# Performance work log

Hardware: AMD Instinct MI355X
Metric: run time of the kernel (lower is better)

The kernel has to match this reference:

```python
import jax, jax.numpy as jnp
import numpy as np

D_MODEL = 1024
NUM_HEADS = 16
D_K = D_MODEL // NUM_HEADS
B, S = 4, 2048


def setup_inputs() -> dict:
    key = jax.random.key(0)
    ks = jax.random.split(key, 11)
    scale = 1.0 / np.sqrt(D_MODEL)
    inp = {
        "query": jax.random.normal(ks[0], (B, S, D_MODEL), dtype=jnp.float32),
        "key": jax.random.normal(ks[1], (B, S, D_MODEL), dtype=jnp.float32),
        "value": jax.random.normal(ks[2], (B, S, D_MODEL), dtype=jnp.float32),
        "w_q": jax.random.normal(ks[3], (D_MODEL, D_MODEL), dtype=jnp.float32) * scale,
        "b_q": jnp.zeros((D_MODEL,), dtype=jnp.float32),
        "w_k": jax.random.normal(ks[4], (D_MODEL, D_MODEL), dtype=jnp.float32) * scale,
        "b_k": jnp.zeros((D_MODEL,), dtype=jnp.float32),
        "w_v": jax.random.normal(ks[5], (D_MODEL, D_MODEL), dtype=jnp.float32) * scale,
        "b_v": jnp.zeros((D_MODEL,), dtype=jnp.float32),
        "w_o": jax.random.normal(ks[6], (D_MODEL, D_MODEL), dtype=jnp.float32) * scale,
        "b_o": jnp.zeros((D_MODEL,), dtype=jnp.float32),
    }
    return inp


def reference(query, key, value, w_q, b_q, w_k, b_k, w_v, b_v, w_o, b_o):
    # Linear projections; torch Linear computes x @ W.T + b, here w_* stored as (out, in)
    def proj(x, w, b):
        y = jnp.einsum("bsd,ed->bse", x, w) + b
        # [B, S, D] -> [B, H, S, d_k]
        return y.reshape(B, S, NUM_HEADS, D_K).transpose(0, 2, 1, 3)

    Q = proj(query, w_q, b_q)
    K = proj(key, w_k, b_k)
    V = proj(value, w_v, b_v)

    scores = jnp.einsum("bhqd,bhkd->bhqk", Q, K) / jnp.sqrt(jnp.float32(D_K))
    weights = jax.nn.softmax(scores, axis=-1)
    attn = jnp.einsum("bhqk,bhkd->bhqd", weights, V)  # [B, H, S, d_k]
    attn = attn.transpose(0, 2, 1, 3).reshape(B, S, D_MODEL)
    return jnp.einsum("bsd,ed->bse", attn, w_o) + b_o
```

## Files before the change

kernel.cpp:

```cpp
#include <hip/hip_runtime.h>
#include <hip/hip_bf16.h>

#define D_MODEL 1024
#define NHEADS 16
#define DKH 64
#define BATCH 4
#define SEQ 2048
#define MROWS (BATCH*SEQ)
#define BSD ((size_t)MROWS * D_MODEL)
#define WSZ ((size_t)D_MODEL * D_MODEL)
#define LOG2E 1.4426950408889634f
#define NT2 (SEQ/32)

typedef __attribute__((ext_vector_type(8)))  short   s16x8;
typedef __attribute__((ext_vector_type(8)))  __bf16  bf16x8;
typedef __attribute__((ext_vector_type(4)))  __bf16  bf16x4;
typedef __attribute__((ext_vector_type(4)))  float   f32x4;
typedef __attribute__((ext_vector_type(16))) float   f32x16;

#define SWZ(row, scol) ((((int)(row)) << 6) + (((int)(scol)) ^ ((((int)(row)) & 7) << 3)))
#define SWZV(row, scol) ((((int)(row)) << 5) + (((int)(scol)) ^ (((((int)(row)) >> 1) & 3) << 3)))

__device__ inline short f2bf(float f) {
    __bf16 h = (__bf16)f;
    short s; __builtin_memcpy(&s, &h, 2); return s;
}

__device__ inline unsigned pk2(float a, float b) {
    unsigned r;
    asm("v_cvt_pk_bf16_f32 %0, %1, %2" : "=v"(r) : "v"(a), "v"(b));
    return r;
}
__device__ inline bf16x8 mk8(unsigned w0, unsigned w1, unsigned w2, unsigned w3) {
    union { unsigned u[4]; bf16x8 v; } x;
    x.u[0] = w0; x.u[1] = w1; x.u[2] = w2; x.u[3] = w3;
    return x.v;
}

__device__ inline void gl_lds16(const void* g, void* l) {
    __builtin_amdgcn_global_load_lds(
        (const __attribute__((address_space(1))) unsigned*)g,
        (__attribute__((address_space(3))) unsigned*)l, 16, 0, 0);
}

struct CvtPtrs { const float* src[7]; short* dst[7]; };

__global__ __launch_bounds__(256) void cvt_all(CvtPtrs p)
{
    const int bx = blockIdx.x;
    int buf, boff;
    if (bx < 3 * 4096) { buf = bx >> 12; boff = bx & 4095; }
    else { const int r = bx - 3 * 4096; buf = 3 + (r >> 9); boff = r & 511; }
    const float* __restrict__ src = p.src[buf];
    short* __restrict__ dst = p.dst[buf];
    const size_t i = ((size_t)boff * 256 + threadIdx.x) * 8;
    const float4 a = *(const float4*)(src + i);
    const float4 b = *(const float4*)(src + i + 4);
    s16x8 v;
    v[0]=f2bf(a.x); v[1]=f2bf(a.y); v[2]=f2bf(a.z); v[3]=f2bf(a.w);
    v[4]=f2bf(b.x); v[5]=f2bf(b.y); v[6]=f2bf(b.z); v[7]=f2bf(b.w);
    *(s16x8*)(dst + i) = v;
}

__device__ __forceinline__ void gemm_body(
    const short* __restrict__ A, const short* __restrict__ W,
    const float* __restrict__ bias, void* __restrict__ Cout, float scale,
    int omode)
{
    __shared__ __align__(16) short As[128 * 64];
    __shared__ __align__(16) short Bs[128 * 64];
    const int t   = threadIdx.x;
    const int l   = t & 63;
    const int wid = t >> 6;
    const int g   = l >> 4, r16 = l & 15;
    const int wm  = wid >> 1, wn = wid & 1;
    const int bid = blockIdx.x + (blockIdx.y << 3);
    const int swz = (bid & 7) * 64 + (bid >> 3);
    const int n0  = (swz & 7) * 128, m0 = (swz >> 3) * 128;
    const int srow = t >> 3;
    const int scol = (t & 7) * 8;

    f32x4 acc[4][4];
    #pragma unroll
    for (int mi = 0; mi < 4; ++mi)
        #pragma unroll
        for (int ni = 0; ni < 4; ++ni)
            acc[mi][ni] = (f32x4)0.0f;

    const short* Ap = A + (size_t)(m0 + srow) * D_MODEL + scol;
    const short* Wp = W + (size_t)(n0 + srow) * D_MODEL + scol;
    short* AsW = As + wid * 512;
    short* BsW = Bs + wid * 512;

    for (int k0 = 0; k0 < D_MODEL; k0 += 64) {
        #pragma unroll
        for (int p = 0; p < 4; ++p) {
            gl_lds16(Ap + (size_t)p * 32 * D_MODEL + k0, AsW + p * 2048);
            gl_lds16(Wp + (size_t)p * 32 * D_MODEL + k0, BsW + p * 2048);
        }
        __syncthreads();
        #pragma unroll
        for (int kc = 0; kc < 2; ++kc) {
            bf16x8 a[4], b[4];
            #pragma unroll
            for (int mi = 0; mi < 4; ++mi)
                a[mi] = *(const bf16x8*)&As[(wm * 64 + mi * 16 + r16) * 64 + kc * 32 + g * 8];
            #pragma unroll
            for (int ni = 0; ni < 4; ++ni)
                b[ni] = *(const bf16x8*)&Bs[(wn * 64 + ni * 16 + r16) * 64 + kc * 32 + g * 8];
            #pragma unroll
            for (int mi = 0; mi < 4; ++mi)
                #pragma unroll
                for (int ni = 0; ni < 4; ++ni)
                    acc[mi][ni] = __builtin_amdgcn_mfma_f32_16x16x32_bf16(a[mi], b[ni], acc[mi][ni], 0, 0, 0);
        }
        __syncthreads();
    }

    #pragma unroll
    for (int mi = 0; mi < 4; ++mi)
        #pragma unroll
        for (int ni = 0; ni < 4; ++ni) {
            const int n  = n0 + wn * 64 + ni * 16 + r16;
            const int mB = m0 + wm * 64 + mi * 16 + g * 4;
            float v[4];
            #pragma unroll
            for (int j = 0; j < 4; ++j)
                v[j] = (acc[mi][ni][j] + bias[n]) * scale;
            if (omode == 0) {
                #pragma unroll
                for (int j = 0; j < 4; ++j)
                    ((float*)Cout)[(size_t)(mB + j) * D_MODEL + n] = v[j];
            } else if (omode == 1) {
                const size_t base = ((size_t)((mB >> 11) * NHEADS + (n >> 6)) << 11);
                #pragma unroll
                for (int j = 0; j < 4; ++j)
                    ((short*)Cout)[(base + ((mB + j) & 2047)) * DKH + (n & 63)] = f2bf(v[j]);
            } else {
                bf16x4 ov;
                ov[0] = (__bf16)v[0]; ov[1] = (__bf16)v[1];
                ov[2] = (__bf16)v[2]; ov[3] = (__bf16)v[3];
                const size_t row = (size_t)((mB >> 11) * NHEADS + (n >> 6)) * DKH + (n & 63);
                *(bf16x4*)&((short*)Cout)[row * SEQ + (mB & 2047)] = ov;
            }
        }
}

struct QkvArgs {
    const short* A[3]; const short* W[3]; const float* bias[3];
    short* out[3]; float scale[3]; int omode[3];
};

__global__ __launch_bounds__(256, 2) void gemm_qkv(QkvArgs q) {
    const int z = blockIdx.z;
    gemm_body(q.A[z], q.W[z], q.bias[z], q.out[z], q.scale[z], q.omode[z]);
}

__global__ __launch_bounds__(256, 2) void gemm_out(
    const short* A, const short* W, const float* bias, float* C) {
    gemm_body(A, W, bias, C, 1.0f, 0);
}

__global__ __launch_bounds__(256, 2) void attn_mfma(
    const short* __restrict__ Qg, const short* __restrict__ Kg,
    const short* __restrict__ Vtg, short* __restrict__ Ab)
{
    __shared__ __align__(16) short lds[24576];
    const int t   = threadIdx.x;
    const int l   = t & 63;
    const int wid = t >> 6;
    const int l31 = l & 31, hi = l >> 5;
    const int bid  = blockIdx.x + (blockIdx.y << 3);
    const int swz  = (bid & 7) * 64 + (bid >> 3);
    const int head = swz >> 3, b = head >> 4, h = head & 15;
    const int q0   = (swz & 7) << 8;
    const int wq0  = wid * 64;

    const short* Kbase = Kg  + (size_t)head * SEQ * DKH;
    const short* Vbase = Vtg + (size_t)head * DKH * SEQ;

    const int qrow = t >> 3;
    const int qg8  = ((t & 7) ^ (qrow & 7)) * 8;
    const short* qsrc = Qg + ((size_t)head * SEQ + q0 + qrow) * DKH + qg8;
    const int krow = t >> 3;
    const short* ksrc = Kbase + (size_t)krow * DKH + (((t & 7) ^ (krow & 7)) * 8);
    const int vrow = t >> 2;
    const short* vsrc = Vbase + (size_t)vrow * SEQ + (((t & 3) ^ ((vrow >> 1) & 3)) * 8);

    short* const ldsQ  = &lds[wid * 512];
    short* const ldsKA = &lds[16384 + wid * 512];
    short* const ldsVA = &lds[18432 + wid * 512];
    short* const ldsKB = &lds[20480 + wid * 512];
    short* const ldsVB = &lds[22528 + wid * 512];

    #pragma unroll
    for (int i = 0; i < 8; ++i)
        gl_lds16(qsrc + (size_t)i * 32 * DKH, ldsQ + i * 2048);
    gl_lds16(ksrc, ldsKA);
    gl_lds16(vsrc, ldsVA);
    gl_lds16(ksrc + 2048, ldsKB);
    gl_lds16(vsrc + 32,   ldsVB);
    __syncthreads();

    bf16x8 bq0[4], bq1[4];
    #pragma unroll
    for (int kc = 0; kc < 4; ++kc) {
        bq0[kc] = *(const bf16x8*)&lds[SWZ(wq0 + l31,      kc * 16 + hi * 8)];
        bq1[kc] = *(const bf16x8*)&lds[SWZ(wq0 + 32 + l31, kc * 16 + hi * 8)];
    }

    f32x16 o00 = (f32x16)0.0f, o01 = (f32x16)0.0f;
    f32x16 o10 = (f32x16)0.0f, o11 = (f32x16)0.0f;
    float l0 = 0.0f, l1 = 0.0f;

    for (int kt = 0; kt < NT2; ++kt) {
        const int KO = (kt & 1) ? 20480 : 16384;
        const int VO = (kt & 1) ? 22528 : 18432;

        f32x16 s0 = (f32x16)0.0f, s1 = (f32x16)0.0f;
        __builtin_amdgcn_s_setprio(1);
        #pragma unroll
        for (int kc = 0; kc < 4; ++kc) {
            const bf16x8 ak = *(const bf16x8*)&lds[KO + SWZ(l31, kc * 16 + hi * 8)];
            s0 = __builtin_amdgcn_mfma_f32_32x32x16_bf16(ak, bq0[kc], s0, 0, 0, 0);
            s1 = __builtin_amdgcn_mfma_f32_32x32x16_bf16(ak, bq1[kc], s1, 0, 0, 0);
        }
        __builtin_amdgcn_s_setprio(0);

        #pragma unroll
        for (int r = 0; r < 16; ++r) s0[r] = __builtin_amdgcn_exp2f(s0[r]);
        #pragma unroll
        for (int r = 0; r < 16; ++r) s1[r] = __builtin_amdgcn_exp2f(s1[r]);
        {
            const float a0 = (s0[0]+s0[1]) + (s0[2]+s0[3]);
            const float a1 = (s0[4]+s0[5]) + (s0[6]+s0[7]);
            const float a2 = (s0[8]+s0[9]) + (s0[10]+s0[11]);
            const float a3 = (s0[12]+s0[13]) + (s0[14]+s0[15]);
            l0 += (a0 + a1) + (a2 + a3);
            const float c0 = (s1[0]+s1[1]) + (s1[2]+s1[3]);
            const float c1 = (s1[4]+s1[5]) + (s1[6]+s1[7]);
            const float c2 = (s1[8]+s1[9]) + (s1[10]+s1[11]);
            const float c3 = (s1[12]+s1[13]) + (s1[14]+s1[15]);
            l1 += (c0 + c1) + (c2 + c3);
        }

        bf16x8 bp00, bp01, bp10, bp11;
        {
            unsigned a0 = pk2(s0[0], s0[1]),  b0 = pk2(s0[4],  s0[5]);
            unsigned a1 = pk2(s0[2], s0[3]),  b1 = pk2(s0[6],  s0[7]);
            asm("v_permlane32_swap_b32 %0, %1" : "+v"(a0), "+v"(b0));
            asm("v_permlane32_swap_b32 %0, %1" : "+v"(a1), "+v"(b1));
            bp00 = mk8(a0, a1, b0, b1);
            unsigned a2 = pk2(s0[8], s0[9]),   b2 = pk2(s0[12], s0[13]);
            unsigned a3 = pk2(s0[10], s0[11]), b3 = pk2(s0[14], s0[15]);
            asm("v_permlane32_swap_b32 %0, %1" : "+v"(a2), "+v"(b2));
            asm("v_permlane32_swap_b32 %0, %1" : "+v"(a3), "+v"(b3));
            bp01 = mk8(a2, a3, b2, b3);
        }
        {
            unsigned a0 = pk2(s1[0], s1[1]),  b0 = pk2(s1[4],  s1[5]);
            unsigned a1 = pk2(s1[2], s1[3]),  b1 = pk2(s1[6],  s1[7]);
            asm("v_permlane32_swap_b32 %0, %1" : "+v"(a0), "+v"(b0));
            asm("v_permlane32_swap_b32 %0, %1" : "+v"(a1), "+v"(b1));
            bp10 = mk8(a0, a1, b0, b1);
            unsigned a2 = pk2(s1[8], s1[9]),   b2 = pk2(s1[12], s1[13]);
            unsigned a3 = pk2(s1[10], s1[11]), b3 = pk2(s1[14], s1[15]);
            asm("v_permlane32_swap_b32 %0, %1" : "+v"(a2), "+v"(b2));
            asm("v_permlane32_swap_b32 %0, %1" : "+v"(a3), "+v"(b3));
            bp11 = mk8(a2, a3, b2, b3);
        }

        __builtin_amdgcn_s_setprio(1);
        {
            const bf16x8 avA0 = *(const bf16x8*)&lds[VO + SWZV(l31,      hi * 8)];
            const bf16x8 avA1 = *(const bf16x8*)&lds[VO + SWZV(32 + l31, hi * 8)];
            o00 = __builtin_amdgcn_mfma_f32_32x32x16_bf16(avA0, bp00, o00, 0, 0, 0);
            o01 = __builtin_amdgcn_mfma_f32_32x32x16_bf16(avA1, bp00, o01, 0, 0, 0);
            o10 = __builtin_amdgcn_mfma_f32_32x32x16_bf16(avA0, bp10, o10, 0, 0, 0);
            o11 = __builtin_amdgcn_mfma_f32_32x32x16_bf16(avA1, bp10, o11, 0, 0, 0);
            const bf16x8 avB0 = *(const bf16x8*)&lds[VO + SWZV(l31,      16 + hi * 8)];
            const bf16x8 avB1 = *(const bf16x8*)&lds[VO + SWZV(32 + l31, 16 + hi * 8)];
            o00 = __builtin_amdgcn_mfma_f32_32x32x16_bf16(avB0, bp01, o00, 0, 0, 0);
            o01 = __builtin_amdgcn_mfma_f32_32x32x16_bf16(avB1, bp01, o01, 0, 0, 0);
            o10 = __builtin_amdgcn_mfma_f32_32x32x16_bf16(avB0, bp11, o10, 0, 0, 0);
            o11 = __builtin_amdgcn_mfma_f32_32x32x16_bf16(avB1, bp11, o11, 0, 0, 0);
        }
        __builtin_amdgcn_s_setprio(0);

        __syncthreads();
        if (kt + 2 < NT2) {
            gl_lds16(ksrc + (size_t)(kt + 2) * 2048, (kt & 1) ? ldsKB : ldsKA);
            gl_lds16(vsrc + (kt + 2) * 32,           (kt & 1) ? ldsVB : ldsVA);
        }
    }

    #pragma unroll
    for (int qb = 0; qb < 2; ++qb) {
        const float lr = qb ? l1 : l0;
        const f32x16 oa = qb ? o10 : o00;
        const f32x16 ob = qb ? o11 : o01;
        const float lt = lr + __shfl_xor(lr, 32);
        const float inv = 1.0f / lt;
        const int q = q0 + wq0 + qb * 32 + l31;
        short* Op = Ab + ((size_t)b * SEQ + q) * D_MODEL + h * DKH;
        #pragma unroll
        for (int rr = 0; rr < 4; ++rr) {
            bf16x4 ov;
            ov[0] = (__bf16)(oa[rr*4+0] * inv); ov[1] = (__bf16)(oa[rr*4+1] * inv);
            ov[2] = (__bf16)(oa[rr*4+2] * inv); ov[3] = (__bf16)(oa[rr*4+3] * inv);
            *(bf16x4*)&Op[rr * 8 + hi * 4] = ov;
            bf16x4 ow;
            ow[0] = (__bf16)(ob[rr*4+0] * inv); ow[1] = (__bf16)(ob[rr*4+1] * inv);
            ow[2] = (__bf16)(ob[rr*4+2] * inv); ow[3] = (__bf16)(ob[rr*4+3] * inv);
            *(bf16x4*)&Op[32 + rr * 8 + hi * 4] = ow;
        }
    }
}

extern "C" void kernel_launch(void* const* d_in, const int* in_sizes, int n_in,
                              void* d_out, int out_size, void* d_ws, size_t ws_size,
                              hipStream_t stream) {
    const float* q_in = (const float*)d_in[0];
    const float* k_in = (const float*)d_in[1];
    const float* v_in = (const float*)d_in[2];
    const float* w_q  = (const float*)d_in[3];
    const float* b_q  = (const float*)d_in[4];
    const float* w_k  = (const float*)d_in[5];
    const float* b_k  = (const float*)d_in[6];
    const float* w_v  = (const float*)d_in[7];
    const float* b_v  = (const float*)d_in[8];
    const float* w_o  = (const float*)d_in[9];
    const float* b_o  = (const float*)d_in[10];
    float* out = (float*)d_out;

    short* ws = (short*)d_ws;
    short* Qc = ws;
    short* Kc = ws + BSD;
    short* Vc = ws + 2 * BSD;
    short* Wq = ws + 3 * BSD;
    short* Wk = Wq + WSZ;
    short* Wv = Wk + WSZ;
    short* Wo = Wv + WSZ;
    short* Qb = ws + 3 * BSD + 4 * WSZ;
    short* Kb = Qb + BSD;
    short* Vt = Kb + BSD;
    short* Ab = Kc;

    dim3 blk(256);

    CvtPtrs cp;
    cp.src[0] = q_in; cp.dst[0] = Qc;
    cp.src[1] = k_in; cp.dst[1] = Kc;
    cp.src[2] = v_in; cp.dst[2] = Vc;
    cp.src[3] = w_q;  cp.dst[3] = Wq;
    cp.src[4] = w_k;  cp.dst[4] = Wk;
    cp.src[5] = w_v;  cp.dst[5] = Wv;
    cp.src[6] = w_o;  cp.dst[6] = Wo;
    cvt_all<<<dim3(3 * 4096 + 4 * 512), blk, 0, stream>>>(cp);

    QkvArgs qa;
    qa.A[0] = Qc; qa.W[0] = Wq; qa.bias[0] = b_q; qa.out[0] = Qb; qa.scale[0] = 0.125f * LOG2E; qa.omode[0] = 1;
    qa.A[1] = Kc; qa.W[1] = Wk; qa.bias[1] = b_k; qa.out[1] = Kb; qa.scale[1] = 1.0f;           qa.omode[1] = 1;
    qa.A[2] = Vc; qa.W[2] = Wv; qa.bias[2] = b_v; qa.out[2] = Vt; qa.scale[2] = 1.0f;           qa.omode[2] = 2;
    gemm_qkv<<<dim3(D_MODEL / 128, MROWS / 128, 3), blk, 0, stream>>>(qa);

    attn_mfma<<<dim3(SEQ / 256, BATCH * NHEADS), blk, 0, stream>>>(Qb, Kb, Vt, Ab);

    gemm_out<<<dim3(D_MODEL / 128, MROWS / 128), blk, 0, stream>>>(Ab, Wo, b_o, out);
}
```

Measured before the change: 195.1 us.

## Load K/V MFMA fragments directly from global into registers, drop LDS staging

The attention kernel no longer stages Q, K and V tiles through shared memory with swizzled layouts and a block barrier. Each wave now loads its MFMA operand fragments straight from global memory into registers, software-prefetching the next K/V tile one iteration ahead. This removes the __syncthreads per tile and the LDS traffic. The cost is that all four waves redundantly fetch the same K/V data through L1/L2, and the loads are uncoalesced strided 16-byte reads with only one-tile lookahead.

```diff
diff --git a/kernel.cpp b/kernel.cpp
--- a/kernel.cpp
+++ b/kernel.cpp
@@ -17,9 +17,6 @@
 typedef __attribute__((ext_vector_type(4)))  __bf16  bf16x4;
 typedef __attribute__((ext_vector_type(4)))  float   f32x4;
 typedef __attribute__((ext_vector_type(16))) float   f32x16;
-
-#define SWZ(row, scol) ((((int)(row)) << 6) + (((int)(scol)) ^ ((((int)(row)) & 7) << 3)))
-#define SWZV(row, scol) ((((int)(row)) << 5) + (((int)(scol)) ^ (((((int)(row)) >> 1) & 3) << 3)))
 
 __device__ inline short f2bf(float f) {
     __bf16 h = (__bf16)f;
@@ -165,7 +162,6 @@
     const short* __restrict__ Qg, const short* __restrict__ Kg,
     const short* __restrict__ Vtg, short* __restrict__ Ab)
 {
-    __shared__ __align__(16) short lds[24576];
     const int t   = threadIdx.x;
     const int l   = t & 63;
     const int wid = t >> 6;
@@ -178,54 +174,49 @@
 
     const short* Kbase = Kg  + (size_t)head * SEQ * DKH;
     const short* Vbase = Vtg + (size_t)head * DKH * SEQ;
-
-    const int qrow = t >> 3;
-    const int qg8  = ((t & 7) ^ (qrow & 7)) * 8;
-    const short* qsrc = Qg + ((size_t)head * SEQ + q0 + qrow) * DKH + qg8;
-    const int krow = t >> 3;
-    const short* ksrc = Kbase + (size_t)krow * DKH + (((t & 7) ^ (krow & 7)) * 8);
-    const int vrow = t >> 2;
-    const short* vsrc = Vbase + (size_t)vrow * SEQ + (((t & 3) ^ ((vrow >> 1) & 3)) * 8);
-
-    short* const ldsQ  = &lds[wid * 512];
-    short* const ldsKA = &lds[16384 + wid * 512];
-    short* const ldsVA = &lds[18432 + wid * 512];
-    short* const ldsKB = &lds[20480 + wid * 512];
-    short* const ldsVB = &lds[22528 + wid * 512];
-
-    #pragma unroll
-    for (int i = 0; i < 8; ++i)
-        gl_lds16(qsrc + (size_t)i * 32 * DKH, ldsQ + i * 2048);
-    gl_lds16(ksrc, ldsKA);
-    gl_lds16(vsrc, ldsVA);
-    gl_lds16(ksrc + 2048, ldsKB);
-    gl_lds16(vsrc + 32,   ldsVB);
-    __syncthreads();
+    const short* Qbase = Qg  + ((size_t)head * SEQ + q0 + wq0) * DKH;
 
     bf16x8 bq0[4], bq1[4];
     #pragma unroll
     for (int kc = 0; kc < 4; ++kc) {
-        bq0[kc] = *(const bf16x8*)&lds[SWZ(wq0 + l31,      kc * 16 + hi * 8)];
-        bq1[kc] = *(const bf16x8*)&lds[SWZ(wq0 + 32 + l31, kc * 16 + hi * 8)];
+        bq0[kc] = *(const bf16x8*)&Qbase[(size_t)l31 * DKH + kc * 16 + hi * 8];
+        bq1[kc] = *(const bf16x8*)&Qbase[(size_t)(32 + l31) * DKH + kc * 16 + hi * 8];
     }
+
+    const short* kp  = Kbase + (size_t)l31 * DKH + hi * 8;
+    const short* vp0 = Vbase + (size_t)l31 * SEQ + hi * 8;
+    const short* vp1 = Vbase + (size_t)(32 + l31) * SEQ + hi * 8;
+
+    bf16x8 kf[4], vf[4];
+    #pragma unroll
+    for (int kc = 0; kc < 4; ++kc) kf[kc] = *(const bf16x8*)&kp[kc * 16];
+    vf[0] = *(const bf16x8*)&vp0[0];  vf[1] = *(const bf16x8*)&vp1[0];
+    vf[2] = *(const bf16x8*)&vp0[16]; vf[3] = *(const bf16x8*)&vp1[16];
 
     f32x16 o00 = (f32x16)0.0f, o01 = (f32x16)0.0f;
     f32x16 o10 = (f32x16)0.0f, o11 = (f32x16)0.0f;
     float l0 = 0.0f, l1 = 0.0f;
 
+    #pragma unroll 2
     for (int kt = 0; kt < NT2; ++kt) {
-        const int KO = (kt & 1) ? 20480 : 16384;
-        const int VO = (kt & 1) ? 22528 : 18432;
-
         f32x16 s0 = (f32x16)0.0f, s1 = (f32x16)0.0f;
         __builtin_amdgcn_s_setprio(1);
         #pragma unroll
         for (int kc = 0; kc < 4; ++kc) {
-            const bf16x8 ak = *(const bf16x8*)&lds[KO + SWZ(l31, kc * 16 + hi * 8)];
-            s0 = __builtin_amdgcn_mfma_f32_32x32x16_bf16(ak, bq0[kc], s0, 0, 0, 0);
-            s1 = __builtin_amdgcn_mfma_f32_32x32x16_bf16(ak, bq1[kc], s1, 0, 0, 0);
+            s0 = __builtin_amdgcn_mfma_f32_32x32x16_bf16(kf[kc], bq0[kc], s0, 0, 0, 0);
+            s1 = __builtin_amdgcn_mfma_f32_32x32x16_bf16(kf[kc], bq1[kc], s1, 0, 0, 0);
         }
         __builtin_amdgcn_s_setprio(0);
+
+        const int nt = (kt + 1 < NT2) ? kt + 1 : kt;
+        bf16x8 kn[4], vn[4];
+        {
+            const short* kpn = kp + (size_t)nt * 2048;
+            #pragma unroll
+            for (int kc = 0; kc < 4; ++kc) kn[kc] = *(const bf16x8*)&kpn[kc * 16];
+            vn[0] = *(const bf16x8*)&vp0[nt * 32];      vn[1] = *(const bf16x8*)&vp1[nt * 32];
+            vn[2] = *(const bf16x8*)&vp0[nt * 32 + 16]; vn[3] = *(const bf16x8*)&vp1[nt * 32 + 16];
+        }
 
         #pragma unroll
         for (int r = 0; r < 16; ++r) s0[r] = __builtin_amdgcn_exp2f(s0[r]);
@@ -271,27 +262,18 @@
         }
 
         __builtin_amdgcn_s_setprio(1);
-        {
-            const bf16x8 avA0 = *(const bf16x8*)&lds[VO + SWZV(l31,      hi * 8)];
-            const bf16x8 avA1 = *(const bf16x8*)&lds[VO + SWZV(32 + l31, hi * 8)];
-            o00 = __builtin_amdgcn_mfma_f32_32x32x16_bf16(avA0, bp00, o00, 0, 0, 0);
-            o01 = __builtin_amdgcn_mfma_f32_32x32x16_bf16(avA1, bp00, o01, 0, 0, 0);
-            o10 = __builtin_amdgcn_mfma_f32_32x32x16_bf16(avA0, bp10, o10, 0, 0, 0);
-            o11 = __builtin_amdgcn_mfma_f32_32x32x16_bf16(avA1, bp10, o11, 0, 0, 0);
-            const bf16x8 avB0 = *(const bf16x8*)&lds[VO + SWZV(l31,      16 + hi * 8)];
-            const bf16x8 avB1 = *(const bf16x8*)&lds[VO + SWZV(32 + l31, 16 + hi * 8)];
-            o00 = __builtin_amdgcn_mfma_f32_32x32x16_bf16(avB0, bp01, o00, 0, 0, 0);
-            o01 = __builtin_amdgcn_mfma_f32_32x32x16_bf16(avB1, bp01, o01, 0, 0, 0);
-            o10 = __builtin_amdgcn_mfma_f32_32x32x16_bf16(avB0, bp11, o10, 0, 0, 0);
-            o11 = __builtin_amdgcn_mfma_f32_32x32x16_bf16(avB1, bp11, o11, 0, 0, 0);
-        }
+        o00 = __builtin_amdgcn_mfma_f32_32x32x16_bf16(vf[0], bp00, o00, 0, 0, 0);
+        o01 = __builtin_amdgcn_mfma_f32_32x32x16_bf16(vf[1], bp00, o01, 0, 0, 0);
+        o10 = __builtin_amdgcn_mfma_f32_32x32x16_bf16(vf[0], bp10, o10, 0, 0, 0);
+        o11 = __builtin_amdgcn_mfma_f32_32x32x16_bf16(vf[1], bp10, o11, 0, 0, 0);
+        o00 = __builtin_amdgcn_mfma_f32_32x32x16_bf16(vf[2], bp01, o00, 0, 0, 0);
+        o01 = __builtin_amdgcn_mfma_f32_32x32x16_bf16(vf[3], bp01, o01, 0, 0, 0);
+        o10 = __builtin_amdgcn_mfma_f32_32x32x16_bf16(vf[2], bp11, o10, 0, 0, 0);
+        o11 = __builtin_amdgcn_mfma_f32_32x32x16_bf16(vf[3], bp11, o11, 0, 0, 0);
         __builtin_amdgcn_s_setprio(0);
 
-        __syncthreads();
-        if (kt + 2 < NT2) {
-            gl_lds16(ksrc + (size_t)(kt + 2) * 2048, (kt & 1) ? ldsKB : ldsKA);
-            gl_lds16(vsrc + (kt + 2) * 32,           (kt & 1) ? ldsVB : ldsVA);
-        }
+        #pragma unroll
+        for (int kc = 0; kc < 4; ++kc) { kf[kc] = kn[kc]; vf[kc] = vn[kc]; }
     }
 
     #pragma unroll
```

New measurement: 237.9 us. 1.22x slower.

## Fuse activation bf16 conversion into QKV GEMM loading fp32 tiles directly

Applied to the files above, without the earlier changes.

Drops the standalone fp32-to-bf16 conversion of query/key/value and has the QKV GEMM load fp32 tiles into LDS via direct global-to-LDS loads, converting to bf16 with packed conversions when forming MFMA operands. This removes a full read/write pass over the activations and the intermediate buffers. It costs double-size A tiles in LDS and extra conversion instructions in the inner loop, and the output GEMM is split into its own specialized kernel.

```diff
diff --git a/kernel.cpp b/kernel.cpp
--- a/kernel.cpp
+++ b/kernel.cpp
@@ -43,14 +43,12 @@
         (__attribute__((address_space(3))) unsigned*)l, 16, 0, 0);
 }
 
-struct CvtPtrs { const float* src[7]; short* dst[7]; };
-
-__global__ __launch_bounds__(256) void cvt_all(CvtPtrs p)
+struct CvtPtrs { const float* src[4]; short* dst[4]; };
+
+__global__ __launch_bounds__(256) void cvt_w(CvtPtrs p)
 {
     const int bx = blockIdx.x;
-    int buf, boff;
-    if (bx < 3 * 4096) { buf = bx >> 12; boff = bx & 4095; }
-    else { const int r = bx - 3 * 4096; buf = 3 + (r >> 9); boff = r & 511; }
+    const int buf = bx >> 9, boff = bx & 511;
     const float* __restrict__ src = p.src[buf];
     short* __restrict__ dst = p.dst[buf];
     const size_t i = ((size_t)boff * 256 + threadIdx.x) * 8;
@@ -62,10 +60,108 @@
     *(s16x8*)(dst + i) = v;
 }
 
-__device__ __forceinline__ void gemm_body(
+struct QkvArgs {
+    const float* A[3]; const short* W[3]; const float* bias[3];
+    short* out[3]; float scale[3]; int omode[3];
+};
+
+__global__ __launch_bounds__(256, 2) void gemm_qkv(QkvArgs qa)
+{
+    __shared__ __align__(16) float Af[128 * 64];
+    __shared__ __align__(16) short Bs[128 * 64];
+    const int z   = blockIdx.z;
+    const float* __restrict__ A = qa.A[z];
+    const short* __restrict__ W = qa.W[z];
+    const float* __restrict__ bias = qa.bias[z];
+    short* __restrict__ Cout = qa.out[z];
+    const float scale = qa.scale[z];
+    const int omode = qa.omode[z];
+
+    const int t   = threadIdx.x;
+    const int l   = t & 63;
+    const int wid = t >> 6;
+    const int g   = l >> 4, r16 = l & 15;
+    const int wm  = wid >> 1, wn = wid & 1;
+    const int bid = blockIdx.x + (blockIdx.y << 3);
+    const int swz = (bid & 7) * 64 + (bid >> 3);
+    const int n0  = (swz & 7) * 128, m0 = (swz >> 3) * 128;
+
+    f32x4 acc[4][4];
+    #pragma unroll
+    for (int mi = 0; mi < 4; ++mi)
+        #pragma unroll
+        for (int ni = 0; ni < 4; ++ni)
+            acc[mi][ni] = (f32x4)0.0f;
+
+    const int arow = t >> 4;
+    const int acol = (((t & 15) ^ (arow & 7)) << 2);
+    const float* Ap = A + (size_t)(m0 + arow) * D_MODEL + acol;
+    float* AfW = Af + wid * 256;
+    const int brow = t >> 3;
+    const int bcol = (t & 7) * 8;
+    const short* Wp = W + (size_t)(n0 + brow) * D_MODEL + bcol;
+    short* BsW = Bs + wid * 512;
+
+    for (int k0 = 0; k0 < D_MODEL; k0 += 64) {
+        #pragma unroll
+        for (int p = 0; p < 8; ++p)
+            gl_lds16(Ap + (size_t)p * 16 * D_MODEL + k0, AfW + p * 1024);
+        #pragma unroll
+        for (int p = 0; p < 4; ++p)
+            gl_lds16(Wp + (size_t)p * 32 * D_MODEL + k0, BsW + p * 2048);
+        __syncthreads();
+        #pragma unroll
+        for (int kc = 0; kc < 2; ++kc) {
+            bf16x8 a[4], b[4];
+            #pragma unroll
+            for (int mi = 0; mi < 4; ++mi) {
+                const int row = wm * 64 + mi * 16 + r16;
+                const int rx  = r16 & 7;
+                const int c4  = kc * 8 + g * 2;
+                const float4 x = *(const float4*)&Af[row * 64 + ((c4 ^ rx) << 2)];
+                const float4 y = *(const float4*)&Af[row * 64 + (((c4 + 1) ^ rx) << 2)];
+                a[mi] = mk8(pk2(x.x, x.y), pk2(x.z, x.w), pk2(y.x, y.y), pk2(y.z, y.w));
+            }
+            #pragma unroll
+            for (int ni = 0; ni < 4; ++ni)
+                b[ni] = *(const bf16x8*)&Bs[(wn * 64 + ni * 16 + r16) * 64 + kc * 32 + g * 8];
+            #pragma unroll
+            for (int mi = 0; mi < 4; ++mi)
+                #pragma unroll
+                for (int ni = 0; ni < 4; ++ni)
+                    acc[mi][ni] = __builtin_amdgcn_mfma_f32_16x16x32_bf16(a[mi], b[ni], acc[mi][ni], 0, 0, 0);
+        }
+        __syncthreads();
+    }
+
+    #pragma unroll
+    for (int mi = 0; mi < 4; ++mi)
+        #pragma unroll
+        for (int ni = 0; ni < 4; ++ni) {
+            const int n  = n0 + wn * 64 + ni * 16 + r16;
+            const int mB = m0 + wm * 64 + mi * 16 + g * 4;
+            float v[4];
+            #pragma unroll
+            for (int j = 0; j < 4; ++j)
+                v[j] = (acc[mi][ni][j] + bias[n]) * scale;
+            if (omode == 1) {
+                const size_t base = ((size_t)((mB >> 11) * NHEADS + (n >> 6)) << 11);
+                #pragma unroll
+                for (int j = 0; j < 4; ++j)
+                    Cout[(base + ((mB + j) & 2047)) * DKH + (n & 63)] = f2bf(v[j]);
+            } else {
+                bf16x4 ov;
+                ov[0] = (__bf16)v[0]; ov[1] = (__bf16)v[1];
+                ov[2] = (__bf16)v[2]; ov[3] = (__bf16)v[3];
+                const size_t row = (size_t)((mB >> 11) * NHEADS + (n >> 6)) * DKH + (n & 63);
+                *(bf16x4*)&Cout[row * SEQ + (mB & 2047)] = ov;
+            }
+        }
+}
+
+__global__ __launch_bounds__(256, 2) void gemm_out(
     const short* __restrict__ A, const short* __restrict__ W,
-    const float* __restrict__ bias, void* __restrict__ Cout, float scale,
-    int omode)
+    const float* __restrict__ bias, float* __restrict__ C)
 {
     __shared__ __align__(16) short As[128 * 64];
     __shared__ __align__(16) short Bs[128 * 64];
@@ -120,45 +216,13 @@
     #pragma unroll
     for (int mi = 0; mi < 4; ++mi)
         #pragma unroll
-        for (int ni = 0; ni < 4; ++ni) {
-            const int n  = n0 + wn * 64 + ni * 16 + r16;
-            const int mB = m0 + wm * 64 + mi * 16 + g * 4;
-            float v[4];
-            #pragma unroll
-            for (int j = 0; j < 4; ++j)
-                v[j] = (acc[mi][ni][j] + bias[n]) * scale;
-            if (omode == 0) {
-                #pragma unroll
-                for (int j = 0; j < 4; ++j)
-                    ((float*)Cout)[(size_t)(mB + j) * D_MODEL + n] = v[j];
-            } else if (omode == 1) {
-                const size_t base = ((size_t)((mB >> 11) * NHEADS + (n >> 6)) << 11);
-                #pragma unroll
-                for (int j = 0; j < 4; ++j)
-                    ((short*)Cout)[(base + ((mB + j) & 2047)) * DKH + (n & 63)] = f2bf(v[j]);
-            } else {
-                bf16x4 ov;
-                ov[0] = (__bf16)v[0]; ov[1] = (__bf16)v[1];
-                ov[2] = (__bf16)v[2]; ov[3] = (__bf16)v[3];
-                const size_t row = (size_t)((mB >> 11) * NHEADS + (n >> 6)) * DKH + (n & 63);
-                *(bf16x4*)&((short*)Cout)[row * SEQ + (mB & 2047)] = ov;
+        for (int ni = 0; ni < 4; ++ni)
+            #pragma unroll
+            for (int j = 0; j < 4; ++j) {
+                const int m = m0 + wm * 64 + mi * 16 + g * 4 + j;
+                const int n = n0 + wn * 64 + ni * 16 + r16;
+                C[(size_t)m * D_MODEL + n] = acc[mi][ni][j] + bias[n];
             }
-        }
-}
-
-struct QkvArgs {
-    const short* A[3]; const short* W[3]; const float* bias[3];
-    short* out[3]; float scale[3]; int omode[3];
-};
-
-__global__ __launch_bounds__(256, 2) void gemm_qkv(QkvArgs q) {
-    const int z = blockIdx.z;
-    gemm_body(q.A[z], q.W[z], q.bias[z], q.out[z], q.scale[z], q.omode[z]);
-}
-
-__global__ __launch_bounds__(256, 2) void gemm_out(
-    const short* A, const short* W, const float* bias, float* C) {
-    gemm_body(A, W, bias, C, 1.0f, 0);
 }
 
 __global__ __launch_bounds__(256, 2) void attn_mfma(
@@ -334,34 +398,28 @@
     float* out = (float*)d_out;
 
     short* ws = (short*)d_ws;
-    short* Qc = ws;
-    short* Kc = ws + BSD;
-    short* Vc = ws + 2 * BSD;
-    short* Wq = ws + 3 * BSD;
+    short* Wq = ws;
     short* Wk = Wq + WSZ;
     short* Wv = Wk + WSZ;
     short* Wo = Wv + WSZ;
-    short* Qb = ws + 3 * BSD + 4 * WSZ;
+    short* Qb = ws + 4 * WSZ;
     short* Kb = Qb + BSD;
     short* Vt = Kb + BSD;
-    short* Ab = Kc;
+    short* Ab = Vt + BSD;
 
     dim3 blk(256);
 
     CvtPtrs cp;
-    cp.src[0] = q_in; cp.dst[0] = Qc;
-    cp.src[1] = k_in; cp.dst[1] = Kc;
-    cp.src[2] = v_in; cp.dst[2] = Vc;
-    cp.src[3] = w_q;  cp.dst[3] = Wq;
-    cp.src[4] = w_k;  cp.dst[4] = Wk;
-    cp.src[5] = w_v;  cp.dst[5] = Wv;
-    cp.src[6] = w_o;  cp.dst[6] = Wo;
-    cvt_all<<<dim3(3 * 4096 + 4 * 512), blk, 0, stream>>>(cp);
+    cp.src[0] = w_q; cp.dst[0] = Wq;
+    cp.src[1] = w_k; cp.dst[1] = Wk;
+    cp.src[2] = w_v; cp.dst[2] = Wv;
+    cp.src[3] = w_o; cp.dst[3] = Wo;
+    cvt_w<<<dim3(4 * 512), blk, 0, stream>>>(cp);
 
     QkvArgs qa;
-    qa.A[0] = Qc; qa.W[0] = Wq; qa.bias[0] = b_q; qa.out[0] = Qb; qa.scale[0] = 0.125f * LOG2E; qa.omode[0] = 1;
-    qa.A[1] = Kc; qa.W[1] = Wk; qa.bias[1] = b_k; qa.out[1] = Kb; qa.scale[1] = 1.0f;           qa.omode[1] = 1;
-    qa.A[2] = Vc; qa.W[2] = Wv; qa.bias[2] = b_v; qa.out[2] = Vt; qa.scale[2] = 1.0f;           qa.omode[2] = 2;
+    qa.A[0] = q_in; qa.W[0] = Wq; qa.bias[0] = b_q; qa.out[0] = Qb; qa.scale[0] = 0.125f * LOG2E; qa.omode[0] = 1;
+    qa.A[1] = k_in; qa.W[1] = Wk; qa.bias[1] = b_k; qa.out[1] = Kb; qa.scale[1] = 1.0f;           qa.omode[1] = 1;
+    qa.A[2] = v_in; qa.W[2] = Wv; qa.bias[2] = b_v; qa.out[2] = Vt; qa.scale[2] = 1.0f;           qa.omode[2] = 2;
     gemm_qkv<<<dim3(D_MODEL / 128, MROWS / 128, 3), blk, 0, stream>>>(qa);
 
     attn_mfma<<<dim3(SEQ / 256, BATCH * NHEADS), blk, 0, stream>>>(Qb, Kb, Vt, Ab);
```

After: 192.5 us. About the same (-1.3%).
